# Kernel optimization log

Hardware: AMD Instinct MI355X
Metric: run time of the kernel (lower is better)

Reference implementation:

```python
import jax, jax.numpy as jnp
import numpy as np

H = 256
B = 4096          # number of graphs / motifs in batch
NF = 131072       # focal atoms
NR = 262144       # residues
V = 8001          # vocab.size() + 1
TOPK = 5
DIST_THRESH = 6.0


def setup_inputs() -> dict:
    key = jax.random.key(0)
    ks = jax.random.split(key, 12)
    h_ctx_focal = jax.random.normal(ks[0], (NF, H), dtype=jnp.float32)
    pos_ctx_focal = jax.random.normal(ks[1], (NF, 3), dtype=jnp.float32)
    current_wid = jax.random.randint(ks[2], (B,), 0, V)
    current_atoms_batch = jnp.sort(jax.random.randint(ks[3], (NF,), 0, B))
    h_residue = jax.random.normal(ks[4], (NR, H), dtype=jnp.float32)
    residue_pos = jax.random.normal(ks[5], (NR, 3, 3), dtype=jnp.float32)
    amino_acid_batch = jnp.sort(jax.random.randint(ks[6], (NR,), 0, B))
    emb_weight = jax.random.normal(ks[7], (V, H), dtype=jnp.float32) * 0.02
    mlp_w1 = jax.random.normal(ks[8], (3 * H, H), dtype=jnp.float32) * (1.0 / np.sqrt(3 * H))
    mlp_b1 = jnp.zeros((H,), dtype=jnp.float32)
    mlp_w2 = jax.random.normal(ks[9], (H, H), dtype=jnp.float32) * (1.0 / np.sqrt(H))
    mlp_b2 = jnp.zeros((H,), dtype=jnp.float32)
    return {
        'h_ctx_focal': h_ctx_focal, 'pos_ctx_focal': pos_ctx_focal,
        'current_wid': current_wid, 'current_atoms_batch': current_atoms_batch,
        'h_residue': h_residue, 'residue_pos': residue_pos,
        'amino_acid_batch': amino_acid_batch, 'emb_weight': emb_weight,
        'mlp_w1': mlp_w1, 'mlp_b1': mlp_b1, 'mlp_w2': mlp_w2, 'mlp_b2': mlp_b2,
    }


def reference(h_ctx_focal, pos_ctx_focal, current_wid, current_atoms_batch,
              h_residue, residue_pos, amino_acid_batch,
              emb_weight, mlp_w1, mlp_b1, mlp_w2, mlp_b2):
    nB = current_wid.shape[0]
    # scatter_add over focal atoms -> [B, H]
    node_hiddens = jax.ops.segment_sum(h_ctx_focal, current_atoms_batch, num_segments=nB)
    # embedding lookup -> [B, H]
    motif_hiddens = emb_weight[current_wid]
    # scatter_mean of positions -> [B, 3]
    pos_sum = jax.ops.segment_sum(pos_ctx_focal, current_atoms_batch, num_segments=nB)
    counts = jax.ops.segment_sum(jnp.ones((pos_ctx_focal.shape[0],), jnp.float32),
                                 current_atoms_batch, num_segments=nB)
    center_pos = pos_sum / jnp.maximum(counts, 1.0)[:, None]
    # CA position of each residue, distance mask (< 6 A from motif center)
    ca_pos = residue_pos[:, 1, :]                                  # [NR, 3]
    dist = jnp.linalg.norm(ca_pos - center_pos[amino_acid_batch], axis=1)
    mask = dist < DIST_THRESH                                      # [NR]
    # masked scatter_add of residue embeddings -> [B, H]
    residue_emb = jax.ops.segment_sum(jnp.where(mask[:, None], h_residue, 0.0),
                                      amino_acid_batch, num_segments=nB)
    # motif MLP (2 layers) + projection onto embedding table
    pred_vecs = jnp.concatenate([node_hiddens, motif_hiddens, residue_emb], axis=-1)  # [B, 3H]
    h = jax.nn.relu(pred_vecs @ mlp_w1 + mlp_b1)
    mh = h @ mlp_w2 + mlp_b2                                        # [B, H]
    pred_scores = mh @ emb_weight.T                                 # [B, V]
    # top-k + random selection among top-k
    _, select_pool = jax.lax.top_k(pred_scores, TOPK)               # [B, k]
    idx = jax.random.randint(jax.random.key(1), (nB,), 0, TOPK)
    preds = jnp.take_along_axis(select_pool, idx[:, None], axis=1)[:, 0]
    return (pred_scores, preds)
```

## Files before the change

### kernel.cpp

```cpp
#include <hip/hip_runtime.h>
#include <hip/hip_bf16.h>
#include <cstdint>

#define HD   256
#define BSZ  4096
#define NFV  131072
#define NRV  262144
#define VV   8001
#define TOPKN 5
#define RBOFF (BSZ + 1)
#define EPAD 8064

typedef __attribute__((ext_vector_type(8))) short short8v;
typedef __attribute__((ext_vector_type(4))) float float4v;

__host__ __device__ __forceinline__ unsigned rotl32(unsigned v, int d) {
  return (v << d) | (v >> (32 - d));
}

__host__ __device__ __forceinline__ void threefry2x32(
    unsigned k0, unsigned k1, unsigned x0, unsigned x1,
    unsigned& o0, unsigned& o1) {
  unsigned ks2 = k0 ^ k1 ^ 0x1BD11BDAu;
  x0 += k0; x1 += k1;
  x0 += x1; x1 = rotl32(x1, 13); x1 ^= x0;
  x0 += x1; x1 = rotl32(x1, 15); x1 ^= x0;
  x0 += x1; x1 = rotl32(x1, 26); x1 ^= x0;
  x0 += x1; x1 = rotl32(x1,  6); x1 ^= x0;
  x0 += k1; x1 += ks2 + 1u;
  x0 += x1; x1 = rotl32(x1, 17); x1 ^= x0;
  x0 += x1; x1 = rotl32(x1, 29); x1 ^= x0;
  x0 += x1; x1 = rotl32(x1, 16); x1 ^= x0;
  x0 += x1; x1 = rotl32(x1, 24); x1 ^= x0;
  x0 += ks2; x1 += k0 + 2u;
  x0 += x1; x1 = rotl32(x1, 13); x1 ^= x0;
  x0 += x1; x1 = rotl32(x1, 15); x1 ^= x0;
  x0 += x1; x1 = rotl32(x1, 26); x1 ^= x0;
  x0 += x1; x1 = rotl32(x1,  6); x1 ^= x0;
  x0 += k0; x1 += k1 + 3u;
  x0 += x1; x1 = rotl32(x1, 17); x1 ^= x0;
  x0 += x1; x1 = rotl32(x1, 29); x1 ^= x0;
  x0 += x1; x1 = rotl32(x1, 16); x1 ^= x0;
  x0 += x1; x1 = rotl32(x1, 24); x1 ^= x0;
  x0 += k1; x1 += ks2 + 4u;
  x0 += x1; x1 = rotl32(x1, 13); x1 ^= x0;
  x0 += x1; x1 = rotl32(x1, 15); x1 ^= x0;
  x0 += x1; x1 = rotl32(x1, 26); x1 ^= x0;
  x0 += x1; x1 = rotl32(x1,  6); x1 ^= x0;
  x0 += ks2; x1 += k0 + 5u;
  o0 = x0; o1 = x1;
}

__device__ __forceinline__ unsigned short f2bf(float f) {
  unsigned u = __float_as_uint(f);
  unsigned r = (u + 0x7FFFu + ((u >> 16) & 1u)) >> 16;
  return (unsigned short)r;
}
__device__ __forceinline__ float bf2f(unsigned short s) {
  return __uint_as_float(((unsigned)s) << 16);
}

__device__ __forceinline__ int lower_bound_i(const int* __restrict__ a, int n, int v) {
  int lo = 0, hi = n;
  while (lo < hi) { int m = (lo + hi) >> 1; if (a[m] < v) lo = m + 1; else hi = m; }
  return lo;
}

__device__ __forceinline__ void gl16(const unsigned short* g, unsigned short* l) {
  __builtin_amdgcn_global_load_lds(
      (const __attribute__((address_space(1))) unsigned int*)g,
      (__attribute__((address_space(3))) unsigned int*)l, 16, 0, 0);
}

__global__ __launch_bounds__(256) void prep_kernel(
    const int* __restrict__ ab, const int* __restrict__ rb, int* __restrict__ bounds,
    const float* __restrict__ emb, unsigned short* __restrict__ ehi,
    unsigned short* __restrict__ elo,
    const float* __restrict__ w1, unsigned short* __restrict__ w1th,
    unsigned short* __restrict__ w1tl,
    const float* __restrict__ w2, unsigned short* __restrict__ w2th,
    unsigned short* __restrict__ w2tl) {
  int blk = blockIdx.x, t = threadIdx.x;
  if (blk < 33) {
    int i = blk * 256 + t;
    if (i <= BSZ) bounds[i] = lower_bound_i(ab, NFV, i);
    else if (i <= 2 * BSZ + 1) bounds[i] = lower_bound_i(rb, NRV, i - RBOFF);
  } else if (blk < 33 + 2016) {
    size_t i = ((size_t)(blk - 33) * 256 + t) * 4;
    int row = (int)(i >> 8);
    float f[4] = {0.f, 0.f, 0.f, 0.f};
    if (row < VV) {
      float4 v = *reinterpret_cast<const float4*>(&emb[i]);
      f[0] = v.x; f[1] = v.y; f[2] = v.z; f[3] = v.w;
    }
    unsigned short h[4], l[4];
#pragma unroll
    for (int j = 0; j < 4; ++j) {
      h[j] = f2bf(f[j]);
      l[j] = f2bf(f[j] - bf2f(h[j]));
    }
    *reinterpret_cast<uint2*>(&ehi[i]) = *reinterpret_cast<uint2*>(h);
    *reinterpret_cast<uint2*>(&elo[i]) = *reinterpret_cast<uint2*>(l);
  } else if (blk < 33 + 2016 + 768) {
    int i = (blk - 2049) * 256 + t;
    int n = i / 768, k = i - n * 768;
    float v = w1[k * 256 + n];
    unsigned short h = f2bf(v);
    w1th[i] = h; w1tl[i] = f2bf(v - bf2f(h));
  } else {
    int i = (blk - 2817) * 256 + t;
    int n = i >> 8, k = i & 255;
    float v = w2[k * 256 + n];
    unsigned short h = f2bf(v);
    w2th[i] = h; w2tl[i] = f2bf(v - bf2f(h));
  }
}

__global__ __launch_bounds__(256) void mask_kernel(
    const float* __restrict__ pcf, const float* __restrict__ rpos,
    const int* __restrict__ bounds, unsigned char* __restrict__ mask) {
  int lane = threadIdx.x & 63;
  int b = blockIdx.x * 4 + (threadIdx.x >> 6);
  int a0 = bounds[b], a1 = bounds[b + 1];
  int r0 = bounds[RBOFF + b], r1 = bounds[RBOFF + b + 1];

  float cp = 0.f;
  if (lane < 3 && a0 < a1) {
    float nv = pcf[(size_t)a0 * 3 + lane];
    for (int aa = a0; aa < a1; ++aa) {
      float cv = nv;
      if (aa + 1 < a1) nv = pcf[(size_t)(aa + 1) * 3 + lane];
      cp += cv;
    }
  }
  if (lane < 3) cp = cp / fmaxf((float)(a1 - a0), 1.0f);
  float cx = __shfl(cp, 0), cy = __shfl(cp, 1), cz = __shfl(cp, 2);

  for (int r = r0 + lane; r < r1; r += 64) {
    float dx = rpos[(size_t)r * 9 + 3] - cx;
    float dy = rpos[(size_t)r * 9 + 4] - cy;
    float dz = rpos[(size_t)r * 9 + 5] - cz;
    mask[r] = (dx * dx + dy * dy + dz * dz < 36.0f) ? 1 : 0;
  }
}

__global__ __launch_bounds__(256) void fuse_seg_kernel(
    const float* __restrict__ hcf, const int* __restrict__ wid,
    const float* __restrict__ hres, const unsigned char* __restrict__ mask,
    const unsigned short* __restrict__ ehi, const unsigned short* __restrict__ elo,
    const int* __restrict__ bounds,
    unsigned short* __restrict__ pvh, unsigned short* __restrict__ pvl) {
  int lane = threadIdx.x & 63;
  int b = blockIdx.x * 4 + (threadIdx.x >> 6);
  int a0 = bounds[b], a1 = bounds[b + 1];
  int r0 = bounds[RBOFF + b], r1 = bounds[RBOFF + b + 1];
  size_t off = (size_t)lane * 4;

  float4v acc = 0.f;
  int a = a0;
  for (; a + 8 <= a1; a += 8) {
    float4v v[8];
#pragma unroll
    for (int j = 0; j < 8; ++j)
      v[j] = *reinterpret_cast<const float4v*>(&hcf[(size_t)(a + j) * HD + off]);
    acc += ((v[0] + v[1]) + (v[2] + v[3])) + ((v[4] + v[5]) + (v[6] + v[7]));
  }
  for (; a < a1; ++a)
    acc += *reinterpret_cast<const float4v*>(&hcf[(size_t)a * HD + off]);

  float4v racc = 0.f;
  int r = r0;
  for (; r < r1 && (r & 7); ++r) {
    float4v v = *reinterpret_cast<const float4v*>(&hres[(size_t)r * HD + off]);
    if (mask[r]) racc += v;
  }
  for (; r + 8 <= r1; r += 8) {
    uint2 mw = *reinterpret_cast<const uint2*>(&mask[r]);
    float4v v[8];
#pragma unroll
    for (int j = 0; j < 8; ++j)
      v[j] = *reinterpret_cast<const float4v*>(&hres[(size_t)(r + j) * HD + off]);
    float4v s0 = 0.f, s1 = 0.f, s2 = 0.f, s3 = 0.f;
    if (mw.x & 0x000000FFu) s0 += v[0];
    if (mw.x & 0x0000FF00u) s1 += v[1];
    if (mw.x & 0x00FF0000u) s2 += v[2];
    if (mw.x & 0xFF000000u) s3 += v[3];
    if (mw.y & 0x000000FFu) s0 += v[4];
    if (mw.y & 0x0000FF00u) s1 += v[5];
    if (mw.y & 0x00FF0000u) s2 += v[6];
    if (mw.y & 0xFF000000u) s3 += v[7];
    racc += (s0 + s1) + (s2 + s3);
  }
  for (; r < r1; ++r) {
    float4v v = *reinterpret_cast<const float4v*>(&hres[(size_t)r * HD + off]);
    if (mask[r]) racc += v;
  }

  size_t o = (size_t)b * 768;
  {
    unsigned short h[4], l[4];
#pragma unroll
    for (int j = 0; j < 4; ++j) {
      h[j] = f2bf(acc[j]); l[j] = f2bf(acc[j] - bf2f(h[j]));
    }
    *reinterpret_cast<uint2*>(&pvh[o + off]) = *reinterpret_cast<uint2*>(h);
    *reinterpret_cast<uint2*>(&pvl[o + off]) = *reinterpret_cast<uint2*>(l);
  }
  *reinterpret_cast<uint2*>(&pvh[o + 256 + off]) =
      *reinterpret_cast<const uint2*>(&ehi[(size_t)wid[b] * 256 + off]);
  *reinterpret_cast<uint2*>(&pvl[o + 256 + off]) =
      *reinterpret_cast<const uint2*>(&elo[(size_t)wid[b] * 256 + off]);
  {
    unsigned short h[4], l[4];
#pragma unroll
    for (int j = 0; j < 4; ++j) {
      h[j] = f2bf(racc[j]); l[j] = f2bf(racc[j] - bf2f(h[j]));
    }
    *reinterpret_cast<uint2*>(&pvh[o + 512 + off]) = *reinterpret_cast<uint2*>(h);
    *reinterpret_cast<uint2*>(&pvl[o + 512 + off]) = *reinterpret_cast<uint2*>(l);
  }
}

template <bool RELU, int K, int N>
__global__ __launch_bounds__(256) void mlp_gemm_kernel(
    const unsigned short* __restrict__ Ahg, const unsigned short* __restrict__ Alg,
    const unsigned short* __restrict__ Bhg, const unsigned short* __restrict__ Blg,
    const float* __restrict__ bias,
    unsigned short* __restrict__ Chi, unsigned short* __restrict__ Clo) {
  __shared__ __attribute__((aligned(16))) unsigned short Ahs[64][72];
  __shared__ __attribute__((aligned(16))) unsigned short Als[64][72];
  __shared__ __attribute__((aligned(16))) unsigned short Bhs[64][72];
  __shared__ __attribute__((aligned(16))) unsigned short Bls[64][72];

  int t = threadIdx.x;
  int bm = blockIdx.y * 64, bn = blockIdx.x * 64;
  int lane = t & 63, wv = t >> 6;
  int wm = wv >> 1, wn = wv & 1;
  int lr = lane & 15, lg = lane >> 4;
  float4v acc[2][2] = {};

  int srow = t >> 2, sc = (t & 3) * 16;

  for (int kb = 0; kb < K; kb += 64) {
    size_t ga = (size_t)(bm + srow) * K + kb + sc;
    size_t gb = (size_t)(bn + srow) * K + kb + sc;
    *reinterpret_cast<short8v*>(&Ahs[srow][sc]) = *reinterpret_cast<const short8v*>(&Ahg[ga]);
    *reinterpret_cast<short8v*>(&Ahs[srow][sc + 8]) = *reinterpret_cast<const short8v*>(&Ahg[ga + 8]);
    *reinterpret_cast<short8v*>(&Als[srow][sc]) = *reinterpret_cast<const short8v*>(&Alg[ga]);
    *reinterpret_cast<short8v*>(&Als[srow][sc + 8]) = *reinterpret_cast<const short8v*>(&Alg[ga + 8]);
    *reinterpret_cast<short8v*>(&Bhs[srow][sc]) = *reinterpret_cast<const short8v*>(&Bhg[gb]);
    *reinterpret_cast<short8v*>(&Bhs[srow][sc + 8]) = *reinterpret_cast<const short8v*>(&Bhg[gb + 8]);
    *reinterpret_cast<short8v*>(&Bls[srow][sc]) = *reinterpret_cast<const short8v*>(&Blg[gb]);
    *reinterpret_cast<short8v*>(&Bls[srow][sc + 8]) = *reinterpret_cast<const short8v*>(&Blg[gb + 8]);
    __syncthreads();

#pragma unroll
    for (int ks = 0; ks < 2; ++ks) {
      int ko = ks * 32 + lg * 8;
      short8v aH[2], aL[2], bH[2], bL[2];
#pragma unroll
      for (int f = 0; f < 2; ++f) {
        aH[f] = *reinterpret_cast<const short8v*>(&Ahs[wm * 32 + f * 16 + lr][ko]);
        aL[f] = *reinterpret_cast<const short8v*>(&Als[wm * 32 + f * 16 + lr][ko]);
        bH[f] = *reinterpret_cast<const short8v*>(&Bhs[wn * 32 + f * 16 + lr][ko]);
        bL[f] = *reinterpret_cast<const short8v*>(&Bls[wn * 32 + f * 16 + lr][ko]);
      }
#pragma unroll
      for (int mf = 0; mf < 2; ++mf)
#pragma unroll
        for (int nf = 0; nf < 2; ++nf) {
          acc[mf][nf] = __builtin_amdgcn_mfma_f32_16x16x32_bf16(
              aH[mf], bH[nf], acc[mf][nf], 0, 0, 0);
          acc[mf][nf] = __builtin_amdgcn_mfma_f32_16x16x32_bf16(
              aH[mf], bL[nf], acc[mf][nf], 0, 0, 0);
          acc[mf][nf] = __builtin_amdgcn_mfma_f32_16x16x32_bf16(
              aL[mf], bH[nf], acc[mf][nf], 0, 0, 0);
        }
    }
    __syncthreads();
  }

#pragma unroll
  for (int mf = 0; mf < 2; ++mf)
#pragma unroll
    for (int nf = 0; nf < 2; ++nf) {
      int col = bn + wn * 32 + nf * 16 + lr;
      float bv = bias[col];
#pragma unroll
      for (int rr = 0; rr < 4; ++rr) {
        int row = bm + wm * 32 + mf * 16 + lg * 4 + rr;
        float v = acc[mf][nf][rr] + bv;
        if (RELU) v = fmaxf(v, 0.f);
        unsigned short h = f2bf(v);
        Chi[(size_t)row * N + col] = h;
        Clo[(size_t)row * N + col] = f2bf(v - bf2f(h));
      }
    }
}

__global__ __launch_bounds__(256, 2) void score_gemm_kernel(
    const unsigned short* __restrict__ Ahg, const unsigned short* __restrict__ Alg,
    const unsigned short* __restrict__ Bhg, const unsigned short* __restrict__ Blg,
    float* __restrict__ C) {
  __shared__ __attribute__((aligned(16))) unsigned short Ah[128 * 64];
  __shared__ __attribute__((aligned(16))) unsigned short Al[128 * 64];
  __shared__ __attribute__((aligned(16))) unsigned short Bh[128 * 64];
  __shared__ __attribute__((aligned(16))) unsigned short Bl[128 * 64];

  int t = threadIdx.x;
  int bm = blockIdx.x * 128;
  int bn = blockIdx.y * 128;
  int lane = t & 63, wv = t >> 6;
  int wm = wv >> 1, wn = wv & 1;
  int lr = lane & 15, lg = lane >> 4;

  float4v acc[4][4] = {};

  int rsub = lane >> 3;
  int csub = (lane & 7) * 8;

  for (int kb = 0; kb < 256; kb += 64) {
#pragma unroll
    for (int j = 0; j < 4; ++j) {
      int ch = wv * 4 + j;
      int grow = ch * 8 + rsub;
      size_t goA = (size_t)(bm + grow) * 256 + kb + csub;
      size_t goB = (size_t)(bn + grow) * 256 + kb + csub;
      unsigned lo = ch * 512 + lane * 8;
      gl16(&Ahg[goA], &Ah[lo]);
      gl16(&Alg[goA], &Al[lo]);
      gl16(&Bhg[goB], &Bh[lo]);
      gl16(&Blg[goB], &Bl[lo]);
    }
    __syncthreads();

#pragma unroll
    for (int ks = 0; ks < 2; ++ks) {
      int ko = ks * 32 + lg * 8;
      short8v aH[4], aL[4], bH[4], bL[4];
#pragma unroll
      for (int f = 0; f < 4; ++f) {
        int ra = wm * 64 + f * 16 + lr;
        int rb2 = wn * 64 + f * 16 + lr;
        aH[f] = *reinterpret_cast<const short8v*>(&Ah[ra * 64 + ko]);
        aL[f] = *reinterpret_cast<const short8v*>(&Al[ra * 64 + ko]);
        bH[f] = *reinterpret_cast<const short8v*>(&Bh[rb2 * 64 + ko]);
        bL[f] = *reinterpret_cast<const short8v*>(&Bl[rb2 * 64 + ko]);
      }
#pragma unroll
      for (int mf = 0; mf < 4; ++mf)
#pragma unroll
        for (int nf = 0; nf < 4; ++nf) {
          acc[mf][nf] = __builtin_amdgcn_mfma_f32_16x16x32_bf16(
              aH[mf], bH[nf], acc[mf][nf], 0, 0, 0);
          acc[mf][nf] = __builtin_amdgcn_mfma_f32_16x16x32_bf16(
              aH[mf], bL[nf], acc[mf][nf], 0, 0, 0);
          acc[mf][nf] = __builtin_amdgcn_mfma_f32_16x16x32_bf16(
              aL[mf], bH[nf], acc[mf][nf], 0, 0, 0);
        }
    }
    __syncthreads();
  }

#pragma unroll
  for (int mf = 0; mf < 4; ++mf)
#pragma unroll
    for (int nf = 0; nf < 4; ++nf) {
      int col = bn + wn * 64 + nf * 16 + lr;
      if (col < VV) {
#pragma unroll
        for (int rr = 0; rr < 4; ++rr) {
          int row = bm + wm * 64 + mf * 16 + lg * 4 + rr;
          C[(size_t)row * VV + col] = acc[mf][nf][rr];
        }
      }
    }
}

#define BETTER(av, ai, bv, bi) ((av) > (bv) || ((av) == (bv) && (ai) < (bi)))

__global__ __launch_bounds__(256) void topk_kernel(
    const float* __restrict__ scores, float* __restrict__ preds,
    unsigned k1a, unsigned k1b, unsigned k2a, unsigned k2b) {
  int lane = threadIdx.x & 63;
  int row = (blockIdx.x << 2) + (threadIdx.x >> 6);
  const float* s = scores + (size_t)row * VV;

  const float NEG = -__builtin_huge_valf();
  float v0 = NEG, v1 = NEG, v2 = NEG, v3 = NEG, v4 = NEG;
  int i0 = 0x7FFFFFFF, i1 = 0x7FFFFFFF, i2 = 0x7FFFFFFF, i3 = 0x7FFFFFFF, i4 = 0x7FFFFFFF;

  for (int v = lane; v < VV; v += 64) {
    float val = s[v];
    if (BETTER(val, v, v4, i4)) {
      if (BETTER(val, v, v3, i3)) {
        v4 = v3; i4 = i3;
        if (BETTER(val, v, v2, i2)) {
          v3 = v2; i3 = i2;
          if (BETTER(val, v, v1, i1)) {
            v2 = v1; i2 = i1;
            if (BETTER(val, v, v0, i0)) {
              v1 = v0; i1 = i0; v0 = val; i0 = v;
            } else { v1 = val; i1 = v; }
          } else { v2 = val; i2 = v; }
        } else { v3 = val; i3 = v; }
      } else { v4 = val; i4 = v; }
    }
  }

  int sel0, sel1, sel2, sel3, sel4;
#pragma unroll
  for (int p = 0; p < TOPKN; ++p) {
    float bv = v0; int bi = i0;
#pragma unroll
    for (int off = 32; off > 0; off >>= 1) {
      float ov = __shfl_xor(bv, off);
      int   oi = __shfl_xor(bi, off);
      if (BETTER(ov, oi, bv, bi)) { bv = ov; bi = oi; }
    }
    if (p == 0) sel0 = bi; else if (p == 1) sel1 = bi; else if (p == 2) sel2 = bi;
    else if (p == 3) sel3 = bi; else sel4 = bi;
    if (bi == i0) {
      v0 = v1; i0 = i1; v1 = v2; i1 = i2; v2 = v3; i2 = i3; v3 = v4; i3 = i4;
      v4 = NEG; i4 = 0x7FFFFFFF;
    }
  }

  if (lane == 0) {
    unsigned i = (unsigned)row;
    unsigned h0, h1, l0, l1;
    threefry2x32(k1a, k1b, 0u, i, h0, h1);
    threefry2x32(k2a, k2b, 0u, i, l0, l1);
    unsigned hb = h0 ^ h1;
    unsigned lb = l0 ^ l1;
    unsigned idx = ((hb % 5u) + (lb % 5u)) % 5u;
    int pick = (idx == 0) ? sel0 : (idx == 1) ? sel1 : (idx == 2) ? sel2
             : (idx == 3) ? sel3 : sel4;
    preds[row] = (float)pick;
  }
}

extern "C" void kernel_launch(void* const* d_in, const int* in_sizes, int n_in,
                              void* d_out, int out_size, void* d_ws, size_t ws_size,
                              hipStream_t stream) {
  const float* hcf  = (const float*)d_in[0];
  const float* pcf  = (const float*)d_in[1];
  const int*   wid  = (const int*)d_in[2];
  const int*   ab   = (const int*)d_in[3];
  const float* hres = (const float*)d_in[4];
  const float* rpos = (const float*)d_in[5];
  const int*   rb   = (const int*)d_in[6];
  const float* emb  = (const float*)d_in[7];
  const float* w1   = (const float*)d_in[8];
  const float* bb1  = (const float*)d_in[9];
  const float* w2   = (const float*)d_in[10];
  const float* bb2  = (const float*)d_in[11];

  float* out    = (float*)d_out;
  float* scores = out;
  float* preds  = out + (size_t)BSZ * VV;

  char* ob = (char*)d_out;
  unsigned short* pvh  = (unsigned short*)(ob);
  unsigned short* pvl  = (unsigned short*)(ob + 0x600000);
  unsigned short* hh   = (unsigned short*)(ob + 0xC00000);
  unsigned short* hl   = (unsigned short*)(ob + 0xE00000);
  unsigned short* w1th = (unsigned short*)(ob + 0x1000000);
  unsigned short* w1tl = (unsigned short*)(ob + 0x1060000);
  unsigned short* w2th = (unsigned short*)(ob + 0x10C0000);
  unsigned short* w2tl = (unsigned short*)(ob + 0x10E0000);

  char* ws = (char*)d_ws;
  int*            bounds = (int*)(ws);
  unsigned char*  mask   = (unsigned char*)(ws + 0x10000);
  unsigned short* mh_hi  = (unsigned short*)(ws + 0x100000);
  unsigned short* mh_lo  = (unsigned short*)(ws + 0x300000);
  unsigned short* emb_hi = (unsigned short*)(ws + 0x500000);
  unsigned short* emb_lo = (unsigned short*)(ws + 0x900000);

  prep_kernel<<<33 + 2016 + 768 + 256, 256, 0, stream>>>(
      ab, rb, bounds, emb, emb_hi, emb_lo, w1, w1th, w1tl, w2, w2th, w2tl);

  mask_kernel<<<BSZ / 4, 256, 0, stream>>>(pcf, rpos, bounds, mask);

  fuse_seg_kernel<<<BSZ / 4, 256, 0, stream>>>(
      hcf, wid, hres, mask, emb_hi, emb_lo, bounds, pvh, pvl);

  mlp_gemm_kernel<true, 768, 256><<<dim3(4, 64), 256, 0, stream>>>(
      pvh, pvl, w1th, w1tl, bb1, hh, hl);
  mlp_gemm_kernel<false, 256, 256><<<dim3(4, 64), 256, 0, stream>>>(
      hh, hl, w2th, w2tl, bb2, mh_hi, mh_lo);

  score_gemm_kernel<<<dim3(BSZ / 128, (VV + 127) / 128), 256, 0, stream>>>(
      mh_hi, mh_lo, emb_hi, emb_lo, scores);

  unsigned k1a, k1b, k2a, k2b;
  threefry2x32(0u, 1u, 0u, 0u, k1a, k1b);
  threefry2x32(0u, 1u, 0u, 1u, k2a, k2b);
  topk_kernel<<<BSZ / 4, 256, 0, stream>>>(scores, preds, k1a, k1b, k2a, k2b);
}
```

Before: 295.9 us.

## Fuse partial top-k into score GEMM epilogue and add merge kernel

The score GEMM epilogue now computes per-row top-5 candidates for each half tile, packing a monotonic float key and the column index into 64 bits, and writes them to workspace. A small merge kernel then reduces 630 candidates per row instead of rescanning the full 8001-wide score row from memory. The GEMM block order is also swizzled so that concurrently running blocks share tiles in cache. The fused path is taken only when the workspace is large enough (about 20 MB of candidates), and the epilogue adds shuffle work and extra writes to the GEMM.

```diff
diff --git a/kernel.cpp b/kernel.cpp
--- a/kernel.cpp
+++ b/kernel.cpp
@@ -10,9 +10,11 @@
 #define TOPKN 5
 #define RBOFF (BSZ + 1)
 #define EPAD 8064
+#define NBN  63
 
 typedef __attribute__((ext_vector_type(8))) short short8v;
 typedef __attribute__((ext_vector_type(4))) float float4v;
+typedef unsigned long long u64;
 
 __host__ __device__ __forceinline__ unsigned rotl32(unsigned v, int d) {
   return (v << d) | (v >> (32 - d));
@@ -60,6 +62,16 @@
   return __uint_as_float(((unsigned)s) << 16);
 }
 
+__device__ __forceinline__ unsigned f2mono(float f) {
+  unsigned u = __float_as_uint(f);
+  return ((int)u < 0) ? ~u : (u | 0x80000000u);
+}
+__device__ __forceinline__ u64 shflx64(u64 v, int off) {
+  int lo = __shfl_xor((int)(unsigned)v, off);
+  int hi = __shfl_xor((int)(unsigned)(v >> 32), off);
+  return ((u64)(unsigned)hi << 32) | (unsigned)lo;
+}
+
 __device__ __forceinline__ int lower_bound_i(const int* __restrict__ a, int n, int v) {
   int lo = 0, hi = n;
   while (lo < hi) { int m = (lo + hi) >> 1; if (a[m] < v) lo = m + 1; else hi = m; }
@@ -301,15 +313,19 @@
 __global__ __launch_bounds__(256, 2) void score_gemm_kernel(
     const unsigned short* __restrict__ Ahg, const unsigned short* __restrict__ Alg,
     const unsigned short* __restrict__ Bhg, const unsigned short* __restrict__ Blg,
-    float* __restrict__ C) {
+    float* __restrict__ C, u64* __restrict__ cand) {
   __shared__ __attribute__((aligned(16))) unsigned short Ah[128 * 64];
   __shared__ __attribute__((aligned(16))) unsigned short Al[128 * 64];
   __shared__ __attribute__((aligned(16))) unsigned short Bh[128 * 64];
   __shared__ __attribute__((aligned(16))) unsigned short Bl[128 * 64];
 
   int t = threadIdx.x;
-  int bm = blockIdx.x * 128;
-  int bn = blockIdx.y * 128;
+  int orig = blockIdx.x + blockIdx.y * gridDim.x;
+  int cpx = (gridDim.x * gridDim.y) >> 3;
+  int swz = (orig & 7) * cpx + (orig >> 3);
+  int bmi = swz % gridDim.x, bni = swz / gridDim.x;
+  int bm = bmi * 128, bn = bni * 128;
+
   int lane = t & 63, wv = t >> 6;
   int wm = wv >> 1, wn = wv & 1;
   int lr = lane & 15, lg = lane >> 4;
@@ -375,6 +391,94 @@
         }
       }
     }
+
+  if (cand) {
+#pragma unroll
+    for (int mf = 0; mf < 4; ++mf)
+#pragma unroll
+      for (int rr = 0; rr < 4; ++rr) {
+        int row = bm + wm * 64 + mf * 16 + lg * 4 + rr;
+        u64 q[4];
+#pragma unroll
+        for (int nf = 0; nf < 4; ++nf) {
+          int col = bn + wn * 64 + nf * 16 + lr;
+          q[nf] = (col < VV)
+              ? (((u64)f2mono(acc[mf][nf][rr]) << 32) | (0xFFFFFFFFu - (unsigned)col))
+              : 0ULL;
+        }
+        u64 s0, s1, s2, s3, s4;
+#pragma unroll
+        for (int p = 0; p < 5; ++p) {
+          u64 m = q[0];
+          if (q[1] > m) m = q[1];
+          if (q[2] > m) m = q[2];
+          if (q[3] > m) m = q[3];
+#pragma unroll
+          for (int off = 1; off < 16; off <<= 1) {
+            u64 o = shflx64(m, off);
+            if (o > m) m = o;
+          }
+          if (p == 0) s0 = m; else if (p == 1) s1 = m; else if (p == 2) s2 = m;
+          else if (p == 3) s3 = m; else s4 = m;
+#pragma unroll
+          for (int nf = 0; nf < 4; ++nf)
+            if (q[nf] == m) q[nf] = 0ULL;
+        }
+        if (lr < 5) {
+          u64 v = (lr == 0) ? s0 : (lr == 1) ? s1 : (lr == 2) ? s2
+                : (lr == 3) ? s3 : s4;
+          size_t base = (((size_t)row * NBN + bni) * 2 + wn) * 5;
+          cand[base + lr] = v;
+        }
+      }
+  }
+}
+
+__global__ __launch_bounds__(256) void merge_topk_kernel(
+    const u64* __restrict__ cand, float* __restrict__ preds,
+    unsigned k1a, unsigned k1b, unsigned k2a, unsigned k2b) {
+  int lane = threadIdx.x & 63;
+  int row = (blockIdx.x << 2) + (threadIdx.x >> 6);
+  const u64* c = cand + (size_t)row * (NBN * 2 * 5);
+
+  u64 q0 = 0, q1 = 0, q2 = 0, q3 = 0, q4 = 0;
+  for (int i = lane; i < NBN * 2 * 5; i += 64) {
+    u64 k = c[i];
+    if (k > q4) {
+      if (k > q3) { q4 = q3;
+        if (k > q2) { q3 = q2;
+          if (k > q1) { q2 = q1;
+            if (k > q0) { q1 = q0; q0 = k; } else q1 = k;
+          } else q2 = k;
+        } else q3 = k;
+      } else q4 = k;
+    }
+  }
+
+  u64 s0, s1, s2, s3, s4;
+#pragma unroll
+  for (int p = 0; p < 5; ++p) {
+    u64 m = q0;
+#pragma unroll
+    for (int off = 1; off < 64; off <<= 1) {
+      u64 o = shflx64(m, off);
+      if (o > m) m = o;
+    }
+    if (p == 0) s0 = m; else if (p == 1) s1 = m; else if (p == 2) s2 = m;
+    else if (p == 3) s3 = m; else s4 = m;
+    if (m == q0) { q0 = q1; q1 = q2; q2 = q3; q3 = q4; q4 = 0; }
+  }
+
+  if (lane == 0) {
+    unsigned i = (unsigned)row;
+    unsigned h0, h1, l0, l1;
+    threefry2x32(k1a, k1b, 0u, i, h0, h1);
+    threefry2x32(k2a, k2b, 0u, i, l0, l1);
+    unsigned idx = (((h0 ^ h1) % 5u) + ((l0 ^ l1) % 5u)) % 5u;
+    u64 pick = (idx == 0) ? s0 : (idx == 1) ? s1 : (idx == 2) ? s2
+             : (idx == 3) ? s3 : s4;
+    preds[row] = (float)(0xFFFFFFFFu - (unsigned)pick);
+  }
 }
 
 #define BETTER(av, ai, bv, bi) ((av) > (bv) || ((av) == (bv) && (ai) < (bi)))
@@ -431,9 +535,7 @@
     unsigned h0, h1, l0, l1;
     threefry2x32(k1a, k1b, 0u, i, h0, h1);
     threefry2x32(k2a, k2b, 0u, i, l0, l1);
-    unsigned hb = h0 ^ h1;
-    unsigned lb = l0 ^ l1;
-    unsigned idx = ((hb % 5u) + (lb % 5u)) % 5u;
+    unsigned idx = (((h0 ^ h1) % 5u) + ((l0 ^ l1) % 5u)) % 5u;
     int pick = (idx == 0) ? sel0 : (idx == 1) ? sel1 : (idx == 2) ? sel2
              : (idx == 3) ? sel3 : sel4;
     preds[row] = (float)pick;
@@ -477,6 +579,9 @@
   unsigned short* mh_lo  = (unsigned short*)(ws + 0x300000);
   unsigned short* emb_hi = (unsigned short*)(ws + 0x500000);
   unsigned short* emb_lo = (unsigned short*)(ws + 0x900000);
+  u64*            cand   = (u64*)(ws + 0xE00000);
+  size_t need = 0xE00000 + (size_t)BSZ * NBN * 2 * 5 * sizeof(u64);
+  bool fused = (ws_size >= need);
 
   prep_kernel<<<33 + 2016 + 768 + 256, 256, 0, stream>>>(
       ab, rb, bounds, emb, emb_hi, emb_lo, w1, w1th, w1tl, w2, w2th, w2tl);
@@ -492,10 +597,13 @@
       hh, hl, w2th, w2tl, bb2, mh_hi, mh_lo);
 
   score_gemm_kernel<<<dim3(BSZ / 128, (VV + 127) / 128), 256, 0, stream>>>(
-      mh_hi, mh_lo, emb_hi, emb_lo, scores);
+      mh_hi, mh_lo, emb_hi, emb_lo, scores, fused ? cand : nullptr);
 
   unsigned k1a, k1b, k2a, k2b;
   threefry2x32(0u, 1u, 0u, 0u, k1a, k1b);
   threefry2x32(0u, 1u, 0u, 1u, k2a, k2b);
-  topk_kernel<<<BSZ / 4, 256, 0, stream>>>(scores, preds, k1a, k1b, k2a, k2b);
-}
+  if (fused)
+    merge_topk_kernel<<<BSZ / 4, 256, 0, stream>>>(cand, preds, k1a, k1b, k2a, k2b);
+  else
+    topk_kernel<<<BSZ / 4, 256, 0, stream>>>(scores, preds, k1a, k1b, k2a, k2b);
+}
```

Result: slower. 327.5 us (+10.7%).
